# Optimization experiments

Hardware: AMD Instinct MI355X
Metric: run time of the kernel (lower is better)

The kernel has to match this reference:

```python
import jax, jax.numpy as jnp
import numpy as np

B, L, D, H = 16, 512, 1024, 16
DH = D // H
NEG = -1e9  # stands in for -inf mask fill (same softmax result, grad-safe)


def setup_inputs() -> dict:
    key = jax.random.key(0)
    ks = jax.random.split(key, 8)
    x = jax.random.normal(ks[0], (B, L, D), dtype=jnp.float32)
    mask = jnp.ones((B, L), dtype=jnp.int64)
    qmask = jax.random.randint(ks[1], (B, L), 0, 9).astype(jnp.int64)
    # qkv_linear: Linear(D, 4D, bias=False); store as [D, 4D] so y = x @ Wqkv
    Wqkv = jax.random.normal(ks[2], (D, 4 * D), dtype=jnp.float32) / np.sqrt(D)
    # fc: Linear(D, D) with bias; store as [D, D] so y = x @ Wfc + bfc
    Wfc = jax.random.normal(ks[3], (D, D), dtype=jnp.float32) / np.sqrt(D)
    bfc = jnp.zeros((D,), dtype=jnp.float32)
    shift = jnp.abs(jax.random.normal(ks[4], (1,), dtype=jnp.float32)) + 0.001
    bias_p = -jnp.abs(jax.random.normal(ks[5], (1,), dtype=jnp.float32))
    return {"x": x, "mask": mask, "qmask": qmask, "Wqkv": Wqkv,
            "Wfc": Wfc, "bfc": bfc, "shift": shift, "bias_p": bias_p,
            "use_Gaussian": 1}


def reference(x, mask, qmask, Wqkv, Wfc, bfc, shift, bias_p, use_Gaussian):
    b, l, d = x.shape
    qkv = x @ Wqkv                                  # [B, L, 4D]
    q, k1, k2, v = jnp.split(qkv, 4, axis=-1)
    q = q.reshape(b, l, H, DH)                      # [B, L, H, dh]
    k1 = k1.reshape(b, l, H, DH)
    k2 = k2.reshape(b, l, H, DH)
    v = v.reshape(b, l, H, DH)

    attn_self = jnp.einsum('bqhd,bkhd->bhqk', q, k1)    # [B, H, L, L]
    attn_others = jnp.einsum('bqhd,bkhd->bhqk', q, k2)  # [B, H, L, L]

    same = (qmask[:, :, None] == qmask[:, None, :])[:, None]  # [B, 1, L, L]
    attn = jnp.where(same, attn_self, attn_others)  # scale == 1 (scale=False)

    key_valid = (mask != 0)[:, None, None, :]       # [B, 1, 1, L]
    attn = jnp.where(key_valid, attn, NEG)

    if use_Gaussian:
        idx = jnp.arange(l, dtype=jnp.float32)
        sq_dist = (idx[:, None] - idx[None, :]) ** 2        # [L, L]
        dis = -(shift[0] * sq_dist + bias_p[0])
        attn = attn + dis[None, None]

    attn = jax.nn.softmax(attn, axis=-1)            # dropout: eval mode (no-op)
    out = jnp.einsum('bhqk,bkhd->bqhd', attn, v).reshape(b, l, d)
    return out @ Wfc + bfc
```

## Files before the change

### kernel.cpp

```cpp
#include <hip/hip_runtime.h>
#include <hip/hip_bf16.h>

#define B_  16
#define L_  512
#define D_  1024
#define H_  16
#define DH_ 64
#define NEG_ (-1e9f)
#define QB_ 64
#define KB_ 64
#define LDP 72

#define GK  1024
#define NKT 16

typedef unsigned short ushort_t;
typedef __attribute__((ext_vector_type(8))) short bf16x8;
typedef __attribute__((ext_vector_type(4))) float f32x4;

__device__ __forceinline__ ushort_t f2bf(float f) {
    unsigned u = __float_as_uint(f);
    u += 0x7FFFu + ((u >> 16) & 1u);
    return (ushort_t)(u >> 16);
}
__device__ __forceinline__ unsigned packbf(float a, float b) {
    return (unsigned)f2bf(a) | ((unsigned)f2bf(b) << 16);
}

__device__ __forceinline__ void gload_lds16(const void* g, void* l) {
    __builtin_amdgcn_global_load_lds(
        (const __attribute__((address_space(1))) void*)g,
        (__attribute__((address_space(3))) void*)l, 16, 0, 0);
}

__global__ __launch_bounds__(256) void prep_all(const float* __restrict__ x,
                                                const float* __restrict__ Wqkv,
                                                const float* __restrict__ Wfc,
                                                ushort_t* __restrict__ xbf,
                                                ushort_t* __restrict__ WqT,
                                                ushort_t* __restrict__ WfT) {
    __shared__ float tile[32][33];
    const int bid = blockIdx.x;
    const int t   = threadIdx.x;

    if (bid < 8192) {
        const int i = (bid * 256 + t) * 4;
        const float4 v = *(const float4*)&x[i];
        ushort4 o;
        o.x = f2bf(v.x); o.y = f2bf(v.y); o.z = f2bf(v.z); o.w = f2bf(v.w);
        *(ushort4*)&xbf[i] = o;
        return;
    }
    const float* src; ushort_t* dst; int C, gx, gy;
    if (bid < 8192 + 4096) {
        const int lb = bid - 8192;
        src = Wqkv; dst = WqT; C = 4096; gx = lb & 127; gy = lb >> 7;
    } else {
        const int lb = bid - 12288;
        src = Wfc;  dst = WfT; C = 1024; gx = lb & 31;  gy = lb >> 5;
    }
    const int R  = 1024;
    const int r0 = gy * 32, c0 = gx * 32;
    const int tr = t >> 3, tc = (t & 7) * 4;
    const float4 v = *(const float4*)&src[(size_t)(r0 + tr) * C + c0 + tc];
    tile[tr][tc + 0] = v.x;
    tile[tr][tc + 1] = v.y;
    tile[tr][tc + 2] = v.z;
    tile[tr][tc + 3] = v.w;
    __syncthreads();
    ushort4 o;
    o.x = f2bf(tile[tc + 0][tr]);
    o.y = f2bf(tile[tc + 1][tr]);
    o.z = f2bf(tile[tc + 2][tr]);
    o.w = f2bf(tile[tc + 3][tr]);
    *(ushort4*)&dst[(size_t)(c0 + tr) * R + r0 + tc] = o;
}

__global__ __launch_bounds__(256) void gemm_bf16_mfma(const ushort_t* __restrict__ A,
                                                      const ushort_t* __restrict__ Bt,
                                                      const float* __restrict__ bias,
                                                      float* __restrict__ C,
                                                      int M, int N, int K) {
    __shared__ __align__(16) ushort_t As[128 * 64];
    __shared__ __align__(16) ushort_t Bs[128 * 64];

    const int t    = threadIdx.x;
    const int wave = t >> 6;
    const int lane = t & 63;
    const int m0   = blockIdx.y * 128;
    const int n0   = blockIdx.x * 128;
    const int wr   = wave >> 1;
    const int wc   = wave & 1;

    const int lrow = lane >> 3;
    const int ksl  = (lane & 7) ^ lrow;
    const int llo  = lane & 15;
    const int lhi  = lane >> 4;

    f32x4 acc[4][4] = {};

    for (int k0 = 0; k0 < K; k0 += 64) {
        #pragma unroll
        for (int i = 0; i < 4; ++i) {
            const int row = wave * 32 + i * 8;
            gload_lds16(A + (size_t)(m0 + row + lrow) * K + k0 + ksl * 8,
                        As + (size_t)row * 64);
            gload_lds16(Bt + (size_t)(n0 + row + lrow) * K + k0 + ksl * 8,
                        Bs + (size_t)row * 64);
        }
        __syncthreads();

        #pragma unroll
        for (int ks = 0; ks < 2; ++ks) {
            bf16x8 af[4], bfr[4];
            #pragma unroll
            for (int m = 0; m < 4; ++m) {
                const int row = wr * 64 + m * 16 + llo;
                af[m] = *(const bf16x8*)&As[row * 64 + (((ks * 4 + lhi) ^ (row & 7)) << 3)];
            }
            #pragma unroll
            for (int n = 0; n < 4; ++n) {
                const int row = wc * 64 + n * 16 + llo;
                bfr[n] = *(const bf16x8*)&Bs[row * 64 + (((ks * 4 + lhi) ^ (row & 7)) << 3)];
            }
            #pragma unroll
            for (int m = 0; m < 4; ++m)
                #pragma unroll
                for (int n = 0; n < 4; ++n)
                    acc[m][n] = __builtin_amdgcn_mfma_f32_16x16x32_bf16(
                        af[m], bfr[n], acc[m][n], 0, 0, 0);
        }
        __syncthreads();
    }

    #pragma unroll
    for (int m = 0; m < 4; ++m) {
        #pragma unroll
        for (int n = 0; n < 4; ++n) {
            const int col = n0 + wc * 64 + n * 16 + llo;
            const float bv = bias[col];
            #pragma unroll
            for (int i = 0; i < 4; ++i) {
                const int row = m0 + wr * 64 + m * 16 + lhi * 4 + i;
                C[(size_t)row * N + col] = acc[m][n][i] + bv;
            }
        }
    }
}

__global__ __launch_bounds__(512, 2) void gemm128x256(const ushort_t* __restrict__ A,
                                                      const ushort_t* __restrict__ Bt,
                                                      ushort_t* __restrict__ C,
                                                      int nbn, int N) {
    extern __shared__ __align__(16) ushort_t lds[];

    const int t    = threadIdx.x;
    const int wave = t >> 6;
    const int lane = t & 63;
    const int wr   = wave >> 2;
    const int wc   = wave & 3;
    const int lhi  = lane >> 4;
    const int llo  = lane & 15;

    const int cpx = gridDim.x >> 3;
    const int swz = (blockIdx.x & 7) * cpx + (blockIdx.x >> 3);
    const int m0  = (swz / nbn) * 128;
    const int n0  = (swz % nbn) * 256;

    #define STAGE_A(buf, kt)                                                     \
        _Pragma("unroll")                                                        \
        for (int j = 0; j < 2; ++j) {                                            \
            const int row_ = (j * 512 + t) >> 3;                                 \
            const int ks_  = (t & 7) ^ (row_ & 7);                               \
            gload_lds16(A + (size_t)(m0 + row_) * GK + (kt) * 64 + ks_ * 8,      \
                        lds + (buf) * 24576 + j * 4096 + (t >> 6) * 512);        \
        }
    #define STAGE_B(buf, kt)                                                     \
        _Pragma("unroll")                                                        \
        for (int j = 0; j < 4; ++j) {                                            \
            const int row_ = (j * 512 + t) >> 3;                                 \
            const int ks_  = (t & 7) ^ (row_ & 7);                               \
            gload_lds16(Bt + (size_t)(n0 + row_) * GK + (kt) * 64 + ks_ * 8,     \
                        lds + (buf) * 24576 + 8192 + j * 4096 + (t >> 6) * 512); \
        }

    f32x4 acc[4][4] = {};

    STAGE_A(0, 0); STAGE_B(0, 0);
    STAGE_A(1, 1); STAGE_B(1, 1);
    asm volatile("s_waitcnt vmcnt(6)" ::: "memory");
    __builtin_amdgcn_s_barrier();

    for (int kt = 0; kt < NKT; ++kt) {
        const ushort_t* Ab = lds + (kt % 3) * 24576;
        const ushort_t* Bb = Ab + 8192;

        bf16x8 afr[4][2], bfr[4][2];
        #pragma unroll
        for (int mi = 0; mi < 4; ++mi)
            #pragma unroll
            for (int kk = 0; kk < 2; ++kk) {
                const int row = wr * 64 + mi * 16 + llo;
                afr[mi][kk] = *(const bf16x8*)&Ab[row * 64 + (((kk * 4 + lhi) ^ (row & 7)) << 3)];
            }
        #pragma unroll
        for (int n = 0; n < 4; ++n)
            #pragma unroll
            for (int kk = 0; kk < 2; ++kk) {
                const int row = wc * 64 + n * 16 + llo;
                bfr[n][kk] = *(const bf16x8*)&Bb[row * 64 + (((kk * 4 + lhi) ^ (row & 7)) << 3)];
            }

        if (kt + 2 < NKT) { STAGE_A((kt + 2) % 3, kt + 2); STAGE_B((kt + 2) % 3, kt + 2); }

        __builtin_amdgcn_s_setprio(1);
        #pragma unroll
        for (int kk = 0; kk < 2; ++kk)
            #pragma unroll
            for (int mi = 0; mi < 4; ++mi)
                #pragma unroll
                for (int n = 0; n < 4; ++n)
                    acc[mi][n] = __builtin_amdgcn_mfma_f32_16x16x32_bf16(
                        afr[mi][kk], bfr[n][kk], acc[mi][n], 0, 0, 0);
        __builtin_amdgcn_s_setprio(0);

        if (kt + 2 < NKT)      { asm volatile("s_waitcnt vmcnt(6)" ::: "memory"); }
        else if (kt + 1 < NKT) { asm volatile("s_waitcnt vmcnt(0)" ::: "memory"); }
        __builtin_amdgcn_s_barrier();
    }
    #undef STAGE_A
    #undef STAGE_B

    #pragma unroll
    for (int mi = 0; mi < 4; ++mi) {
        #pragma unroll
        for (int n = 0; n < 4; ++n) {
            const int col = n0 + wc * 64 + n * 16 + llo;
            #pragma unroll
            for (int i = 0; i < 4; ++i) {
                const int row = m0 + wr * 64 + mi * 16 + lhi * 4 + i;
                C[(size_t)row * N + col] = f2bf(acc[mi][n][i]);
            }
        }
    }
}

__global__ __launch_bounds__(256) void attn_mfma(const ushort_t* __restrict__ qkv,
                                                 const int* __restrict__ mask,
                                                 const int* __restrict__ qmask,
                                                 const float* __restrict__ shiftp,
                                                 const float* __restrict__ biasp,
                                                 const int* __restrict__ useg,
                                                 ushort_t* __restrict__ O) {
    __shared__ __align__(16) ushort_t K1s[KB_][LDP];
    __shared__ __align__(16) ushort_t K2s[KB_][LDP];
    __shared__ __align__(16) ushort_t Vt[DH_][LDP];
    __shared__ __align__(16) unsigned Ps32[QB_][36];
    __shared__ __align__(16) int      Ms[L_];

    const int t    = threadIdx.x;
    const int wave = t >> 6;
    const int lane = t & 63;
    const int lhi  = lane >> 4;
    const int llo  = lane & 15;

    const int orig = blockIdx.x;
    const int swz  = (orig & 7) * 256 + (orig >> 3);
    const int bh   = swz >> 3;
    const int qb   = swz & 7;
    const int b    = bh >> 4;
    const int h    = bh & 15;
    const int q0   = qb * QB_;

    const float shiftv = shiftp[0];
    const float biasv  = biasp[0];
    const int   useG   = useg[0];
    const size_t rowbase = (size_t)b * L_ * (4 * D_);
    const int    hoff    = h * DH_;

    {
        const int k = t;
        Ms[k]       = (qmask[b * L_ + k] << 1) | (mask[b * L_ + k] != 0 ? 1 : 0);
        Ms[k + 256] = (qmask[b * L_ + k + 256] << 1) | (mask[b * L_ + k + 256] != 0 ? 1 : 0);
    }

    const int gq = q0 + wave * 16 + llo;
    bf16x8 af_q[2];
    #pragma unroll
    for (int ks = 0; ks < 2; ++ks)
        af_q[ks] = *(const bf16x8*)&qkv[rowbase + (size_t)gq * (4 * D_) + hoff
                                        + ks * 32 + lhi * 8];
    const int qm_q = qmask[b * L_ + gq];

    int lo = 0, hi = (L_ / KB_) - 1;
    if (useG) {
        while (lo < hi) {
            const int k0 = lo * KB_;
            int dmin = (k0 > q0) ? (k0 - (q0 + KB_ - 1)) : (q0 - (k0 + KB_ - 1));
            if (dmin < 0) dmin = 0;
            if (shiftv * (float)dmin * (float)dmin > 240.f) ++lo; else break;
        }
        while (hi > lo) {
            const int k0 = hi * KB_;
            int dmin = (k0 > q0) ? (k0 - (q0 + KB_ - 1)) : (q0 - (k0 + KB_ - 1));
            if (dmin < 0) dmin = 0;
            if (shiftv * (float)dmin * (float)dmin > 240.f) --hi; else break;
        }
    }

    float m_run = -1e30f, l_run = 0.f;
    f32x4 acc_o[4] = {};

    const int srow8 = t >> 3;
    const int scol8 = (t & 7) * 8;
    const int vkv   = t & 63;
    const int vd0   = (t >> 6) * 8;

    uint4 pk1[2], pk2[2], pvv[2];

    #define ISSUE_KV(kt_) do {                                                          \
        const int k0_ = (kt_) * KB_;                                                    \
        _Pragma("unroll")                                                               \
        for (int it = 0; it < 2; ++it) {                                                \
            const int row = srow8 + it * 32;                                            \
            const size_t gb = rowbase + (size_t)(k0_ + row) * (4 * D_) + hoff + scol8;  \
            pk1[it] = *(const uint4*)&qkv[gb + D_];                                     \
            pk2[it] = *(const uint4*)&qkv[gb + 2 * D_];                                 \
            const int d_ = vd0 + it * 32;                                               \
            pvv[it] = *(const uint4*)&qkv[rowbase + (size_t)(k0_ + vkv) * (4 * D_)      \
                                          + 3 * D_ + hoff + d_];                        \
        }                                                                               \
    } while (0)

    ISSUE_KV(lo);

    for (int kt = lo; kt <= hi; ++kt) {
        const int k0 = kt * KB_;

        #pragma unroll
        for (int it = 0; it < 2; ++it) {
            const int row = srow8 + it * 32;
            *(uint4*)&K1s[row][scol8] = pk1[it];
            *(uint4*)&K2s[row][scol8] = pk2[it];
            const int d = vd0 + it * 32;
            const uint4 raw = pvv[it];
            Vt[d + 0][vkv] = (ushort_t)(raw.x & 0xFFFFu);
            Vt[d + 1][vkv] = (ushort_t)(raw.x >> 16);
            Vt[d + 2][vkv] = (ushort_t)(raw.y & 0xFFFFu);
            Vt[d + 3][vkv] = (ushort_t)(raw.y >> 16);
            Vt[d + 4][vkv] = (ushort_t)(raw.z & 0xFFFFu);
            Vt[d + 5][vkv] = (ushort_t)(raw.z >> 16);
            Vt[d + 6][vkv] = (ushort_t)(raw.w & 0xFFFFu);
            Vt[d + 7][vkv] = (ushort_t)(raw.w >> 16);
        }
        if (kt < hi) ISSUE_KV(kt + 1);
        __syncthreads();

        f32x4 s1[4], s2[4];
        #pragma unroll
        for (int n = 0; n < 4; ++n) { s1[n] = (f32x4){0,0,0,0}; s2[n] = (f32x4){0,0,0,0}; }
        #pragma unroll
        for (int ks = 0; ks < 2; ++ks) {
            const int kb = ks * 32 + lhi * 8;
            #pragma unroll
            for (int n = 0; n < 4; ++n) {
                const bf16x8 bk1 = *(const bf16x8*)&K1s[n * 16 + llo][kb];
                const bf16x8 bk2 = *(const bf16x8*)&K2s[n * 16 + llo][kb];
                s1[n] = __builtin_amdgcn_mfma_f32_16x16x32_bf16(bk1, af_q[ks], s1[n], 0, 0, 0);
                s2[n] = __builtin_amdgcn_mfma_f32_16x16x32_bf16(bk2, af_q[ks], s2[n], 0, 0, 0);
            }
        }

        float sv[4][4];
        float mx = -1e30f;
        #pragma unroll
        for (int n = 0; n < 4; ++n) {
            const int4 mc = *(const int4*)&Ms[k0 + n * 16 + lhi * 4];
            const int mci[4] = {mc.x, mc.y, mc.z, mc.w};
            #pragma unroll
            for (int i = 0; i < 4; ++i) {
                const int key = k0 + n * 16 + lhi * 4 + i;
                float x = ((mci[i] >> 1) == qm_q) ? s1[n][i] : s2[n][i];
                if (!(mci[i] & 1)) x = NEG_;
                if (useG) {
                    const float dq = (float)(gq - key);
                    x -= shiftv * dq * dq + biasv;
                }
                sv[n][i] = x;
                mx = fmaxf(mx, x);
            }
        }
        mx = fmaxf(mx, __shfl_xor(mx, 16));
        mx = fmaxf(mx, __shfl_xor(mx, 32));

        const float m_new = fmaxf(m_run, mx);
        const float scale = __expf(m_run - m_new);

        float p[4][4], ls = 0.f;
        #pragma unroll
        for (int n = 0; n < 4; ++n)
            #pragma unroll
            for (int i = 0; i < 4; ++i) {
                p[n][i] = __expf(sv[n][i] - m_new);
                ls += p[n][i];
            }
        ls += __shfl_xor(ls, 16);
        ls += __shfl_xor(ls, 32);
        l_run = l_run * scale + ls;
        m_run = m_new;

        #pragma unroll
        for (int n2 = 0; n2 < 4; ++n2) {
            acc_o[n2][0] *= scale; acc_o[n2][1] *= scale;
            acc_o[n2][2] *= scale; acc_o[n2][3] *= scale;
        }

        const int qrow = wave * 16 + llo;
        #pragma unroll
        for (int n = 0; n < 4; ++n) {
            uint2 w;
            w.x = packbf(p[n][0], p[n][1]);
            w.y = packbf(p[n][2], p[n][3]);
            *(uint2*)&Ps32[qrow][n * 8 + lhi * 2] = w;
        }

        #pragma unroll
        for (int ks = 0; ks < 2; ++ks) {
            const int kb = ks * 32 + lhi * 8;
            const bf16x8 bp = *(const bf16x8*)&Ps32[qrow][ks * 16 + lhi * 4];
            #pragma unroll
            for (int n2 = 0; n2 < 4; ++n2) {
                const bf16x8 av = *(const bf16x8*)&Vt[n2 * 16 + llo][kb];
                acc_o[n2] = __builtin_amdgcn_mfma_f32_16x16x32_bf16(av, bp, acc_o[n2], 0, 0, 0);
            }
        }
        __syncthreads();
    }
    #undef ISSUE_KV

    {
        const float inv = 1.f / l_run;
        const int qrow = wave * 16 + llo;
        #pragma unroll
        for (int n2 = 0; n2 < 4; ++n2) {
            uint2 w;
            w.x = packbf(acc_o[n2][0] * inv, acc_o[n2][1] * inv);
            w.y = packbf(acc_o[n2][2] * inv, acc_o[n2][3] * inv);
            *(uint2*)&Ps32[qrow][n2 * 8 + lhi * 2] = w;
        }
    }
    __syncthreads();
    {
        const int row = t >> 2;
        const int c4  = (t & 3) * 8;
        const uint4 a = *(const uint4*)&Ps32[row][c4];
        const uint4 b2 = *(const uint4*)&Ps32[row][c4 + 4];
        ushort_t* dst = &O[(size_t)(b * L_ + q0 + row) * D_ + hoff + c4 * 2];
        *(uint4*)dst       = a;
        *(uint4*)(dst + 8) = b2;
    }
}

extern "C" void kernel_launch(void* const* d_in, const int* in_sizes, int n_in,
                              void* d_out, int out_size, void* d_ws, size_t ws_size,
                              hipStream_t stream) {
    const float* x      = (const float*)d_in[0];
    const int*   mask   = (const int*)d_in[1];
    const int*   qmask  = (const int*)d_in[2];
    const float* Wqkv   = (const float*)d_in[3];
    const float* Wfc    = (const float*)d_in[4];
    const float* bfc    = (const float*)d_in[5];
    const float* shift  = (const float*)d_in[6];
    const float* bias_p = (const float*)d_in[7];
    const int*   useg   = (const int*)d_in[8];
    float*       out    = (float*)d_out;

    const int M  = B_ * L_;
    const int N1 = 4 * D_;

    ushort_t* qkv = (ushort_t*)d_ws;
    ushort_t* Obf = qkv + (size_t)M * N1;
    ushort_t* xbf = Obf + (size_t)M * D_;
    ushort_t* WqT = xbf + (size_t)M * D_;
    ushort_t* WfT = WqT + (size_t)N1 * D_;

    prep_all<<<dim3(8192 + 4096 + 1024), 256, 0, stream>>>(x, Wqkv, Wfc,
                                                           xbf, WqT, WfT);

    gemm128x256<<<dim3(1024), 512, 147456, stream>>>(xbf, WqT, qkv, N1 / 256, N1);

    attn_mfma<<<dim3((B_ * H_) * (L_ / QB_)), 256, 0, stream>>>(qkv, mask, qmask,
                                                                shift, bias_p, useg, Obf);

    gemm_bf16_mfma<<<dim3(D_ / 128, M / 128), 256, 0, stream>>>(
        Obf, WfT, bfc, out, M, D_, D_);
}
```

Before: 176.2 us.

## Rewrite QKV GEMM as 256x256 tile with 8-phase ping-pong pipeline

```diff
diff --git a/kernel.cpp b/kernel.cpp
--- a/kernel.cpp
+++ b/kernel.cpp
@@ -13,6 +13,7 @@
 
 #define GK  1024
 #define NKT 16
+#define NI  8
 
 typedef unsigned short ushort_t;
 typedef __attribute__((ext_vector_type(8))) short bf16x8;
@@ -148,7 +149,7 @@
     }
 }
 
-__global__ __launch_bounds__(512, 2) void gemm128x256(const ushort_t* __restrict__ A,
+__global__ __launch_bounds__(512, 1) void gemm256_8ph(const ushort_t* __restrict__ A,
                                                       const ushort_t* __restrict__ Bt,
                                                       ushort_t* __restrict__ C,
                                                       int nbn, int N) {
@@ -164,81 +165,97 @@
 
     const int cpx = gridDim.x >> 3;
     const int swz = (blockIdx.x & 7) * cpx + (blockIdx.x >> 3);
-    const int m0  = (swz / nbn) * 128;
+    const int m0  = (swz / nbn) * 256;
     const int n0  = (swz % nbn) * 256;
 
-    #define STAGE_A(buf, kt)                                                     \
-        _Pragma("unroll")                                                        \
-        for (int j = 0; j < 2; ++j) {                                            \
-            const int row_ = (j * 512 + t) >> 3;                                 \
-            const int ks_  = (t & 7) ^ (row_ & 7);                               \
-            gload_lds16(A + (size_t)(m0 + row_) * GK + (kt) * 64 + ks_ * 8,      \
-                        lds + (buf) * 24576 + j * 4096 + (t >> 6) * 512);        \
-        }
-    #define STAGE_B(buf, kt)                                                     \
-        _Pragma("unroll")                                                        \
-        for (int j = 0; j < 4; ++j) {                                            \
-            const int row_ = (j * 512 + t) >> 3;                                 \
-            const int ks_  = (t & 7) ^ (row_ & 7);                               \
-            gload_lds16(Bt + (size_t)(n0 + row_) * GK + (kt) * 64 + ks_ * 8,     \
-                        lds + (buf) * 24576 + 8192 + j * 4096 + (t >> 6) * 512); \
-        }
-
-    f32x4 acc[4][4] = {};
-
-    STAGE_A(0, 0); STAGE_B(0, 0);
-    STAGE_A(1, 1); STAGE_B(1, 1);
-    asm volatile("s_waitcnt vmcnt(6)" ::: "memory");
+    #define STAGE(mat, gptr, g0, kt, kh)                                              \
+        _Pragma("unroll")                                                             \
+        for (int j = 0; j < 2; ++j) {                                                 \
+            const int row_ = j * 128 + (t >> 2);                                      \
+            const int sl_  = (t & 3) ^ ((row_ >> 1) & 3);                             \
+            gload_lds16((gptr) + (size_t)((g0) + row_) * GK + (kt) * 64 + (kh) * 32   \
+                            + sl_ * 8,                                                \
+                        lds + (((((kt) & 1) * 2 + (mat)) * 2 + (kh)) * 8192)          \
+                            + (j * 128 + (wave << 4)) * 32);                          \
+        }
+
+    f32x4 acc[8][4] = {};
+    bf16x8 bfr[4];
+
+    #define DO_PHASE(s_, kh_, mh_, READB, STAGE_OPS, ENDWAIT)                          \
+    {                                                                                  \
+        if (READB) {                                                                   \
+            _Pragma("unroll")                                                          \
+            for (int n = 0; n < 4; ++n) {                                              \
+                const int row = wc * 64 + n * 16 + llo;                                \
+                bfr[n] = *(const bf16x8*)&lds[((((s_) * 2 + 1) * 2 + (kh_)) * 8192)    \
+                             + row * 32 + ((lhi ^ ((row >> 1) & 3)) << 3)];            \
+            }                                                                          \
+        }                                                                              \
+        bf16x8 afr[4];                                                                 \
+        _Pragma("unroll")                                                              \
+        for (int mi = 0; mi < 4; ++mi) {                                               \
+            const int row = wr * 128 + ((mh_) * 4 + mi) * 16 + llo;                    \
+            afr[mi] = *(const bf16x8*)&lds[((((s_) * 2 + 0) * 2 + (kh_)) * 8192)       \
+                           + row * 32 + ((lhi ^ ((row >> 1) & 3)) << 3)];              \
+        }                                                                              \
+        STAGE_OPS;                                                                     \
+        __builtin_amdgcn_s_barrier();                                                  \
+        asm volatile("s_waitcnt lgkmcnt(0)" ::: "memory");                             \
+        __builtin_amdgcn_sched_barrier(0);                                             \
+        __builtin_amdgcn_s_setprio(1);                                                 \
+        _Pragma("unroll")                                                              \
+        for (int mi = 0; mi < 4; ++mi)                                                 \
+            _Pragma("unroll")                                                          \
+            for (int n = 0; n < 4; ++n)                                                \
+                acc[(mh_) * 4 + mi][n] = __builtin_amdgcn_mfma_f32_16x16x32_bf16(      \
+                    afr[mi], bfr[n], acc[(mh_) * 4 + mi][n], 0, 0, 0);                 \
+        __builtin_amdgcn_s_setprio(0);                                                 \
+        ENDWAIT;                                                                       \
+        __builtin_amdgcn_s_barrier();                                                  \
+    }
+
+    #define VM(n) asm volatile("s_waitcnt vmcnt(" #n ")" ::: "memory")
+
+    STAGE(1, Bt, n0, 0, 0); STAGE(0, A, m0, 0, 0);
+    STAGE(1, Bt, n0, 0, 1); STAGE(0, A, m0, 0, 1);
+    STAGE(1, Bt, n0, 1, 0); STAGE(0, A, m0, 1, 0);
+    VM(4);
     __builtin_amdgcn_s_barrier();
 
-    for (int kt = 0; kt < NKT; ++kt) {
-        const ushort_t* Ab = lds + (kt % 3) * 24576;
-        const ushort_t* Bb = Ab + 8192;
-
-        bf16x8 afr[4][2], bfr[4][2];
-        #pragma unroll
-        for (int mi = 0; mi < 4; ++mi)
-            #pragma unroll
-            for (int kk = 0; kk < 2; ++kk) {
-                const int row = wr * 64 + mi * 16 + llo;
-                afr[mi][kk] = *(const bf16x8*)&Ab[row * 64 + (((kk * 4 + lhi) ^ (row & 7)) << 3)];
-            }
-        #pragma unroll
-        for (int n = 0; n < 4; ++n)
-            #pragma unroll
-            for (int kk = 0; kk < 2; ++kk) {
-                const int row = wc * 64 + n * 16 + llo;
-                bfr[n][kk] = *(const bf16x8*)&Bb[row * 64 + (((kk * 4 + lhi) ^ (row & 7)) << 3)];
-            }
-
-        if (kt + 2 < NKT) { STAGE_A((kt + 2) % 3, kt + 2); STAGE_B((kt + 2) % 3, kt + 2); }
-
-        __builtin_amdgcn_s_setprio(1);
-        #pragma unroll
-        for (int kk = 0; kk < 2; ++kk)
-            #pragma unroll
-            for (int mi = 0; mi < 4; ++mi)
-                #pragma unroll
-                for (int n = 0; n < 4; ++n)
-                    acc[mi][n] = __builtin_amdgcn_mfma_f32_16x16x32_bf16(
-                        afr[mi][kk], bfr[n][kk], acc[mi][n], 0, 0, 0);
-        __builtin_amdgcn_s_setprio(0);
-
-        if (kt + 2 < NKT)      { asm volatile("s_waitcnt vmcnt(6)" ::: "memory"); }
-        else if (kt + 1 < NKT) { asm volatile("s_waitcnt vmcnt(0)" ::: "memory"); }
-        __builtin_amdgcn_s_barrier();
-    }
-    #undef STAGE_A
-    #undef STAGE_B
+    for (int i = 0; i + 1 < NI; ++i) {
+        const int O = 2 * i + 1;
+        const int E2 = 2 * i + 2, O2 = 2 * i + 3;
+        DO_PHASE(0, 0, 0, 1, { STAGE(1, Bt, n0, O, 1); STAGE(0, A, m0, O, 1); }, )
+        DO_PHASE(0, 0, 1, 0, { STAGE(1, Bt, n0, E2, 0); }, )
+        DO_PHASE(0, 1, 0, 1, { STAGE(0, A, m0, E2, 0); }, )
+        DO_PHASE(0, 1, 1, 0, { }, VM(8))
+        DO_PHASE(1, 0, 0, 1, { STAGE(1, Bt, n0, E2, 1); STAGE(0, A, m0, E2, 1); }, )
+        DO_PHASE(1, 0, 1, 0, { STAGE(1, Bt, n0, O2, 0); }, VM(10))
+        DO_PHASE(1, 1, 0, 1, { STAGE(0, A, m0, O2, 0); }, )
+        DO_PHASE(1, 1, 1, 0, { }, VM(4))
+    }
+    DO_PHASE(0, 0, 0, 1, { STAGE(1, Bt, n0, 15, 1); STAGE(0, A, m0, 15, 1); }, )
+    DO_PHASE(0, 0, 1, 0, { }, )
+    DO_PHASE(0, 1, 0, 1, { }, )
+    DO_PHASE(0, 1, 1, 0, { }, VM(4))
+    DO_PHASE(1, 0, 0, 1, { }, )
+    DO_PHASE(1, 0, 1, 0, { }, VM(0))
+    DO_PHASE(1, 1, 0, 1, { }, )
+    DO_PHASE(1, 1, 1, 0, { }, )
+
+    #undef DO_PHASE
+    #undef STAGE
+    #undef VM
 
     #pragma unroll
-    for (int mi = 0; mi < 4; ++mi) {
+    for (int mi = 0; mi < 8; ++mi) {
         #pragma unroll
         for (int n = 0; n < 4; ++n) {
             const int col = n0 + wc * 64 + n * 16 + llo;
             #pragma unroll
             for (int i = 0; i < 4; ++i) {
-                const int row = m0 + wr * 64 + mi * 16 + lhi * 4 + i;
+                const int row = m0 + wr * 128 + mi * 16 + lhi * 4 + i;
                 C[(size_t)row * N + col] = f2bf(acc[mi][n][i]);
             }
         }
@@ -487,7 +504,8 @@
     prep_all<<<dim3(8192 + 4096 + 1024), 256, 0, stream>>>(x, Wqkv, Wfc,
                                                            xbf, WqT, WfT);
 
-    gemm128x256<<<dim3(1024), 512, 147456, stream>>>(xbf, WqT, qkv, N1 / 256, N1);
+    gemm256_8ph<<<dim3((M / 256) * (N1 / 256)), 512, 131072, stream>>>(
+        xbf, WqT, qkv, N1 / 256, N1);
 
     attn_mfma<<<dim3((B_ * H_) * (L_ / QB_)), 256, 0, stream>>>(qkv, mask, qmask,
                                                                 shift, bias_p, useg, Obf);
```

Result: faster. 168.5 us (-4.4%).
